# Kernel optimization log

Hardware: AMD Instinct MI355X
Metric: run time of the kernel (lower is better)

The kernel has to match this reference:

```python
import jax, jax.numpy as jnp
import numpy as np

D_MODEL = 1024
EXPAND = 2
D_INNER = EXPAND * D_MODEL  # 2048
D_STATE = 16
D_CONV = 4
DT_RANK = D_INNER  # non-int dt_rank resolves to d_inner
BATCH, SEQ = 2, 1024
EPS = 1e-5


def setup_inputs() -> dict:
    key = jax.random.key(0)
    ks = jax.random.split(key, 9)
    s = 0.02
    return {
        "x": jax.random.normal(ks[0], (BATCH, SEQ, D_MODEL), jnp.float32),
        "rms_w": jnp.ones((D_MODEL,), jnp.float32),
        "W_in": jax.random.normal(ks[1], (D_MODEL, 2 * D_INNER), jnp.float32) * s,
        "conv_w": jax.random.normal(ks[2], (D_INNER, 1, D_CONV), jnp.float32) * 0.2,
        "conv_b": jax.random.normal(ks[3], (D_INNER,), jnp.float32) * 0.02,
        "W_x": jax.random.normal(ks[4], (D_INNER, DT_RANK + 2 * D_STATE), jnp.float32) * s,
        "W_dt": jax.random.normal(ks[5], (DT_RANK, D_INNER), jnp.float32) * s,
        "A_log": jax.random.normal(ks[6], (D_INNER, D_STATE), jnp.float32),
        "W_out": jax.random.normal(ks[7], (D_INNER, D_MODEL), jnp.float32) * s,
    }


def _rmsnorm(x, w):
    var = jnp.mean(jnp.square(x), axis=-1, keepdims=True)
    return x * jax.lax.rsqrt(var + EPS) * w


def _forward(x, rms_w, W_in, conv_w, conv_b, W_x, W_dt, A_log, W_out):
    B, L, _ = x.shape
    residual = x
    xn = _rmsnorm(x, rms_w)
    xr = xn @ W_in                                  # [B,L,2*d_inner]
    xs, res = jnp.split(xr, 2, axis=-1)
    # causal depthwise conv1d: torch pads d_conv-1 both sides then slices [:L]
    xc = jnp.transpose(xs, (0, 2, 1))               # [B,d_inner,L]
    xc = jnp.pad(xc, ((0, 0), (0, 0), (D_CONV - 1, 0)))
    xc = jax.lax.conv_general_dilated(
        xc, conv_w, window_strides=(1,), padding='VALID',
        dimension_numbers=('NCH', 'OIH', 'NCH'), feature_group_count=D_INNER)
    xc = xc + conv_b[None, :, None]
    xs = jax.nn.silu(jnp.transpose(xc, (0, 2, 1)))  # [B,L,d_inner]
    x_ssm = xs @ W_x                                # [B,L,d_inner+2*d_state]
    dt, Bm, Cm = jnp.split(x_ssm, [D_INNER, D_INNER + D_STATE], axis=-1)
    dt = jax.nn.softplus(dt @ W_dt)                 # [B,L,d_inner]
    A = -jnp.exp(A_log)                             # [d_inner,d_state]
    A_disc = jnp.exp(A[None, None] * dt[..., None])            # [B,L,d_inner,N]
    Bx = dt[..., None] * Bm[:, :, None, :] * xs[..., None]     # [B,L,d_inner,N]

    def step(h, inp):
        Ad_t, Bx_t, C_t = inp                       # [B,d_inner,N],[B,d_inner,N],[B,N]
        h = Ad_t * h + Bx_t
        y = jnp.einsum('bdn,bn->bd', h, C_t)
        return h, y

    h0 = jnp.zeros((B, D_INNER, D_STATE), xs.dtype)
    _, ys = jax.lax.scan(
        step, h0,
        (jnp.transpose(A_disc, (1, 0, 2, 3)),
         jnp.transpose(Bx, (1, 0, 2, 3)),
         jnp.transpose(Cm, (1, 0, 2))))
    y = jnp.transpose(ys, (1, 0, 2))                # [B,L,d_inner]
    y = y * jax.nn.silu(res)
    out = y @ W_out
    return residual + out


def reference(x, rms_w, W_in, conv_w, conv_b, W_x, W_dt, A_log, W_out):
    return _forward(x, rms_w, W_in, conv_w, conv_b, W_x, W_dt, A_log, W_out)
```

## Files before the change

### kernel.cpp

```cpp
#include <hip/hip_runtime.h>
#include <math.h>

#define B_SZ   2
#define LSEQ   1024
#define DMODEL 1024
#define DINNER 2048
#define DSTATE 16
#define NTOK   (B_SZ * LSEQ)
#define NSSM   (DINNER + 2 * DSTATE)
#define CL     32
#define NCH    (LSEQ / CL)
#define NC     (B_SZ * DINNER)

typedef unsigned short ushort;
typedef __attribute__((ext_vector_type(8))) ushort ushort8;
typedef __attribute__((ext_vector_type(8))) __bf16 bf16x8;
typedef __attribute__((ext_vector_type(4))) float floatx4;

__device__ __forceinline__ float softplus_f(float x) {
  return (x > 20.f) ? x : __logf(1.f + __expf(x));
}
__device__ __forceinline__ float silu_f(float x) {
  return x / (1.f + __expf(-x));
}
__device__ __forceinline__ float bf2f(ushort u) {
  return __uint_as_float(((unsigned)u) << 16);
}
__device__ __forceinline__ ushort f2bf(float f) {
  unsigned u = __float_as_uint(f);
  return (ushort)((u + 0x7FFFu + ((u >> 16) & 1u)) >> 16);
}

__global__ __launch_bounds__(256) void rmsnorm_kernel(
    const float* __restrict__ x, const float* __restrict__ w,
    ushort* __restrict__ xn) {
  int row = blockIdx.x;
  const float* xrow = x + (size_t)row * DMODEL;
  float v[4];
  float ss = 0.f;
#pragma unroll
  for (int i = 0; i < 4; i++) {
    v[i] = xrow[threadIdx.x + 256 * i];
    ss += v[i] * v[i];
  }
  __shared__ float wsum[4];
  int lane = threadIdx.x & 63, wid = threadIdx.x >> 6;
#pragma unroll
  for (int off = 1; off < 64; off <<= 1) ss += __shfl_xor(ss, off);
  if (lane == 0) wsum[wid] = ss;
  __syncthreads();
  float tot = wsum[0] + wsum[1] + wsum[2] + wsum[3];
  float scale = rsqrtf(tot / (float)DMODEL + 1e-5f);
#pragma unroll
  for (int i = 0; i < 4; i++) {
    int j = threadIdx.x + 256 * i;
    xn[(size_t)row * DMODEL + j] = f2bf(v[i] * scale * w[j]);
  }
}

__global__ __launch_bounds__(256) void transpose_w(
    const float* __restrict__ W, ushort* __restrict__ Wt, int K, int N) {
  __shared__ float tile[64][65];
  int n0 = blockIdx.x * 64, k0 = blockIdx.y * 64;
  int c = threadIdx.x & 63, rb = (threadIdx.x >> 6) << 4;
#pragma unroll
  for (int i = 0; i < 16; i++) {
    int k = k0 + rb + i;
    if (k < K && n0 + c < N) tile[rb + i][c] = W[(size_t)k * N + n0 + c];
  }
  __syncthreads();
#pragma unroll
  for (int i = 0; i < 16; i++) {
    int n = n0 + rb + i;
    if (n < N && k0 + c < K)
      Wt[(size_t)n * K + k0 + c] = f2bf(tile[c][rb + i]);
  }
}

__global__ __launch_bounds__(256) void gemm_mfma(
    const ushort* __restrict__ A, int lda,
    const ushort* __restrict__ Bt, int ldb,
    int N, int K, int mode,
    void* __restrict__ C0, void* __restrict__ C1,
    const float* __restrict__ addend) {
  __shared__ ushort As[2 * 128 * 32];
  __shared__ ushort Bs[2 * 128 * 32];
  const int bm = blockIdx.y * 128, bn = blockIdx.x * 128;
  const int tid = threadIdx.x;
  const int wave = tid >> 6, lane = tid & 63;
  const int wm = (wave & 1) << 6, wn = (wave >> 1) << 6;
  const int lrow = lane & 15, quad = lane >> 4;

  const int sr = tid >> 2;
  const int q  = tid & 3;
  const int swr = (sr ^ (sr >> 2)) & 3;
  const int pq = (q ^ swr) << 3;
  const int br0 = min(bn + sr, N - 1);
  const int br1 = min(bn + sr + 64, N - 1);
  const ushort* ga0 = A + (size_t)(bm + sr) * lda + (q << 3);
  const ushort* ga1 = A + (size_t)(bm + sr + 64) * lda + (q << 3);
  const ushort* gb0 = Bt + (size_t)br0 * ldb + (q << 3);
  const ushort* gb1 = Bt + (size_t)br1 * ldb + (q << 3);

  floatx4 acc[4][4];
#pragma unroll
  for (int i = 0; i < 4; i++)
#pragma unroll
    for (int j = 0; j < 4; j++) acc[i][j] = (floatx4){0.f, 0.f, 0.f, 0.f};

  const int swf = ((lrow ^ (lrow >> 2)) & 3);
  const int fq = ((quad ^ swf) << 3);

  const int nk = K >> 5;
  ushort8 ra0 = *(const ushort8*)ga0, ra1 = *(const ushort8*)ga1;
  ushort8 rb0 = *(const ushort8*)gb0, rb1 = *(const ushort8*)gb1;
  for (int kt = 0; kt < nk; kt++) {
    const int bo = (kt & 1) << 12;
    *(ushort8*)&As[bo + sr * 32 + pq] = ra0;
    *(ushort8*)&As[bo + (sr + 64) * 32 + pq] = ra1;
    *(ushort8*)&Bs[bo + sr * 32 + pq] = rb0;
    *(ushort8*)&Bs[bo + (sr + 64) * 32 + pq] = rb1;
    __syncthreads();
    if (kt + 1 < nk) {
      const int ko = (kt + 1) << 5;
      ra0 = *(const ushort8*)(ga0 + ko);
      ra1 = *(const ushort8*)(ga1 + ko);
      rb0 = *(const ushort8*)(gb0 + ko);
      rb1 = *(const ushort8*)(gb1 + ko);
    }
    bf16x8 af[4], bfr[4];
#pragma unroll
    for (int i = 0; i < 4; i++)
      af[i] = __builtin_bit_cast(bf16x8,
          *(const ushort8*)&As[bo + (wm + i * 16 + lrow) * 32 + fq]);
#pragma unroll
    for (int j = 0; j < 4; j++)
      bfr[j] = __builtin_bit_cast(bf16x8,
          *(const ushort8*)&Bs[bo + (wn + j * 16 + lrow) * 32 + fq]);
#pragma unroll
    for (int i = 0; i < 4; i++)
#pragma unroll
      for (int j = 0; j < 4; j++)
        acc[i][j] = __builtin_amdgcn_mfma_f32_16x16x32_bf16(
            af[i], bfr[j], acc[i][j], 0, 0, 0);
  }
  const int m0 = bm + wm, n0 = bn + wn, rq = quad << 2;
#pragma unroll
  for (int i = 0; i < 4; i++) {
#pragma unroll
    for (int j = 0; j < 4; j++) {
#pragma unroll
      for (int r = 0; r < 4; r++) {
        int m = m0 + i * 16 + rq + r;
        int n = n0 + j * 16 + lrow;
        if (n >= N) continue;
        float v = acc[i][j][r];
        if (mode == 0) {
          ((float*)C0)[(size_t)m * N + n] = v + addend[(size_t)m * N + n];
        } else if (mode == 1) {
          if (n < DINNER)
            ((ushort*)C0)[(size_t)m * DINNER + n] = f2bf(v);
          else
            ((ushort*)C1)[(size_t)m * DINNER + n - DINNER] = f2bf(silu_f(v));
        } else if (mode == 2) {
          ((ushort*)C0)[(size_t)m * NSSM + n] = f2bf(v);
          if (n >= DINNER)
            ((float*)C1)[(size_t)m * 32 + n - DINNER] = v;
        } else {
          ((float*)C0)[(size_t)m * DINNER + n] = softplus_f(v);
        }
      }
    }
  }
}

__global__ __launch_bounds__(256) void conv_silu_kernel(
    const ushort* __restrict__ xsraw, const float* __restrict__ cw,
    const float* __restrict__ cb, ushort* __restrict__ xs) {
  int gid = blockIdx.x * 256 + threadIdx.x;
  int c = gid & (DINNER - 1);
  int t = gid >> 11;
  int l = t & (LSEQ - 1);
  float w0 = cw[c * 4 + 0], w1 = cw[c * 4 + 1], w2 = cw[c * 4 + 2], w3 = cw[c * 4 + 3];
  const ushort* col = xsraw + (size_t)t * DINNER + c;
  float acc = cb[c] + w3 * bf2f(col[0]);
  if (l >= 1) acc += w2 * bf2f(col[-DINNER]);
  if (l >= 2) acc += w1 * bf2f(col[-2 * DINNER]);
  if (l >= 3) acc += w0 * bf2f(col[-3 * DINNER]);
  xs[gid] = f2bf(silu_f(acc));
}

__global__ __launch_bounds__(256) void scan_chunk1(
    const float* __restrict__ dt, const ushort* __restrict__ xs,
    const float* __restrict__ bc, const float* __restrict__ A_log,
    float* __restrict__ Bc, float* __restrict__ S) {
  int blk = blockIdx.x;
  int b = blk >> 8;
  int rem = blk & 255;
  int ch = rem >> 3;
  int dblk = rem & 7;
  int d = dblk * 256 + threadIdx.x;
  int c = b * DINNER + d;
  float a[DSTATE];
#pragma unroll
  for (int i = 0; i < 4; i++) {
    float4 v = *(const float4*)(A_log + (size_t)d * DSTATE + 4 * i);
    a[4 * i + 0] = -__expf(v.x);
    a[4 * i + 1] = -__expf(v.y);
    a[4 * i + 2] = -__expf(v.z);
    a[4 * i + 3] = -__expf(v.w);
  }
  float h[DSTATE] = {};
  float Ssum = 0.f;
  size_t t = (size_t)b * LSEQ + (size_t)ch * CL;
#pragma unroll 2
  for (int l = 0; l < CL; l++, t++) {
    float dtv = dt[t * DINNER + d];
    float dx = dtv * bf2f(xs[t * DINNER + d]);
    const float4* Bp = (const float4*)(bc + t * 32);
    float4 b0 = Bp[0], b1 = Bp[1], b2 = Bp[2], b3 = Bp[3];
    float bb[DSTATE] = {b0.x, b0.y, b0.z, b0.w, b1.x, b1.y, b1.z, b1.w,
                        b2.x, b2.y, b2.z, b2.w, b3.x, b3.y, b3.z, b3.w};
#pragma unroll
    for (int n = 0; n < DSTATE; n++)
      h[n] = __expf(a[n] * dtv) * h[n] + dx * bb[n];
    Ssum += dtv;
  }
  float4* outp = (float4*)(Bc + ((size_t)c * NCH + ch) * DSTATE);
  outp[0] = make_float4(h[0], h[1], h[2], h[3]);
  outp[1] = make_float4(h[4], h[5], h[6], h[7]);
  outp[2] = make_float4(h[8], h[9], h[10], h[11]);
  outp[3] = make_float4(h[12], h[13], h[14], h[15]);
  S[c * NCH + ch] = Ssum;
}

__global__ __launch_bounds__(256) void scan_combine(
    const float* __restrict__ A_log, const float* __restrict__ S,
    float* BcHin) {
  int gid = blockIdx.x * 256 + threadIdx.x;
  int c = gid >> 4, n = gid & 15;
  int d = c & (DINNER - 1);
  float a = -__expf(A_log[d * DSTATE + n]);
  float h = 0.f;
  size_t base = (size_t)c * (NCH * DSTATE) + n;
  for (int ch = 0; ch < NCH; ch++) {
    float bcv = BcHin[base + (size_t)ch * DSTATE];
    float decay = __expf(a * S[c * NCH + ch]);
    BcHin[base + (size_t)ch * DSTATE] = h;
    h = decay * h + bcv;
  }
}

__global__ __launch_bounds__(256) void scan_chunk2(
    const float* __restrict__ dt, const ushort* __restrict__ xs,
    const float* __restrict__ bc, const ushort* __restrict__ gate,
    const float* __restrict__ A_log, const float* __restrict__ hin,
    ushort* __restrict__ y) {
  int blk = blockIdx.x;
  int b = blk >> 8;
  int rem = blk & 255;
  int ch = rem >> 3;
  int dblk = rem & 7;
  int d = dblk * 256 + threadIdx.x;
  int c = b * DINNER + d;
  float a[DSTATE];
#pragma unroll
  for (int i = 0; i < 4; i++) {
    float4 v = *(const float4*)(A_log + (size_t)d * DSTATE + 4 * i);
    a[4 * i + 0] = -__expf(v.x);
    a[4 * i + 1] = -__expf(v.y);
    a[4 * i + 2] = -__expf(v.z);
    a[4 * i + 3] = -__expf(v.w);
  }
  float h[DSTATE];
  const float4* hi = (const float4*)(hin + ((size_t)c * NCH + ch) * DSTATE);
#pragma unroll
  for (int i = 0; i < 4; i++) {
    float4 v = hi[i];
    h[4 * i + 0] = v.x; h[4 * i + 1] = v.y; h[4 * i + 2] = v.z; h[4 * i + 3] = v.w;
  }
  size_t t = (size_t)b * LSEQ + (size_t)ch * CL;
#pragma unroll 2
  for (int l = 0; l < CL; l++, t++) {
    float dtv = dt[t * DINNER + d];
    float dx = dtv * bf2f(xs[t * DINNER + d]);
    const float4* Bp = (const float4*)(bc + t * 32);
    const float4* Cp = (const float4*)(bc + t * 32 + 16);
    float4 b0 = Bp[0], b1 = Bp[1], b2 = Bp[2], b3 = Bp[3];
    float4 c0 = Cp[0], c1 = Cp[1], c2 = Cp[2], c3 = Cp[3];
    float bb[DSTATE] = {b0.x, b0.y, b0.z, b0.w, b1.x, b1.y, b1.z, b1.w,
                        b2.x, b2.y, b2.z, b2.w, b3.x, b3.y, b3.z, b3.w};
    float cc[DSTATE] = {c0.x, c0.y, c0.z, c0.w, c1.x, c1.y, c1.z, c1.w,
                        c2.x, c2.y, c2.z, c2.w, c3.x, c3.y, c3.z, c3.w};
    float ysum = 0.f;
#pragma unroll
    for (int n = 0; n < DSTATE; n++) {
      h[n] = __expf(a[n] * dtv) * h[n] + dx * bb[n];
      ysum = fmaf(h[n], cc[n], ysum);
    }
    y[t * DINNER + d] = f2bf(ysum * bf2f(gate[t * DINNER + d]));
  }
}

extern "C" void kernel_launch(void* const* d_in, const int* in_sizes, int n_in,
                              void* d_out, int out_size, void* d_ws, size_t ws_size,
                              hipStream_t stream) {
  const float* x      = (const float*)d_in[0];
  const float* rms_w  = (const float*)d_in[1];
  const float* W_in   = (const float*)d_in[2];
  const float* conv_w = (const float*)d_in[3];
  const float* conv_b = (const float*)d_in[4];
  const float* W_x    = (const float*)d_in[5];
  const float* W_dt   = (const float*)d_in[6];
  const float* A_log  = (const float*)d_in[7];
  const float* W_out  = (const float*)d_in[8];
  float* out = (float*)d_out;

  char* w = (char*)d_ws;
  ushort* xnb   = (ushort*)(w + 0);
  ushort* xsraw = (ushort*)(w + 4194304);
  ushort* gate  = (ushort*)(w + 12582912);
  ushort* xsb   = (ushort*)(w + 20971520);
  ushort* ssmb  = (ushort*)(w + 29360128);
  float*  dtb   = (float*)(w + 37879808);
  ushort* yb    = (ushort*)(w + 54657024);
  ushort* WinT  = (ushort*)(w + 63045632);
  ushort* WxT   = (ushort*)(w + 71434240);
  ushort* WdtT  = (ushort*)(w + 79953920);
  ushort* WoutT = (ushort*)(w + 88342528);
  float* bc = (float*)(w + 0);
  float* S  = (float*)(w + 262144);
  float* Bc = (float*)(w + 4194304);

  transpose_w<<<dim3(64, 16), 256, 0, stream>>>(W_in, WinT, DMODEL, 4096);
  transpose_w<<<dim3(33, 32), 256, 0, stream>>>(W_x, WxT, DINNER, NSSM);
  transpose_w<<<dim3(32, 32), 256, 0, stream>>>(W_dt, WdtT, DINNER, DINNER);
  transpose_w<<<dim3(16, 32), 256, 0, stream>>>(W_out, WoutT, DINNER, DMODEL);

  rmsnorm_kernel<<<NTOK, 256, 0, stream>>>(x, rms_w, xnb);
  gemm_mfma<<<dim3(32, 16), 256, 0, stream>>>(
      xnb, DMODEL, WinT, DMODEL, 4096, DMODEL, 1, xsraw, gate, nullptr);
  conv_silu_kernel<<<(NTOK * DINNER) / 256, 256, 0, stream>>>(xsraw, conv_w, conv_b, xsb);
  gemm_mfma<<<dim3(17, 16), 256, 0, stream>>>(
      xsb, DINNER, WxT, DINNER, NSSM, DINNER, 2, ssmb, bc, nullptr);
  gemm_mfma<<<dim3(16, 16), 256, 0, stream>>>(
      ssmb, NSSM, WdtT, DINNER, DINNER, DINNER, 3, dtb, nullptr, nullptr);
  scan_chunk1<<<B_SZ * NCH * 8, 256, 0, stream>>>(dtb, xsb, bc, A_log, Bc, S);
  scan_combine<<<(NC * DSTATE) / 256, 256, 0, stream>>>(A_log, S, Bc);
  scan_chunk2<<<B_SZ * NCH * 8, 256, 0, stream>>>(dtb, xsb, bc, gate, A_log, Bc, yb);
  gemm_mfma<<<dim3(8, 16), 256, 0, stream>>>(
      yb, DINNER, WoutT, DINNER, DMODEL, DINNER, 0, out, nullptr, x);
}
```

Before: 384.9 us.

## Split-K output GEMM, deepen GEMM K-tile, halve scan chunk, merge weight transposes

Several independent changes land together. The four weight-transpose launches become one kernel dispatched by block index. The GEMM now stages a 64-wide K slice per iteration (two 32-wide sub-tiles, doubling LDS use) with launch bounds targeting two blocks per CU. The final W_out GEMM is split along K across blockIdx.z, writing partials that a separate reduce kernel sums together with the residual. The scan chunk length halves so more blocks run in parallel. The cost is an extra partial buffer round trip, an extra launch, and more chunk state for the combine pass; workspace offsets are reshuffled to make room.

```diff
diff --git a/kernel.cpp b/kernel.cpp
--- a/kernel.cpp
+++ b/kernel.cpp
@@ -8,7 +8,7 @@
 #define DSTATE 16
 #define NTOK   (B_SZ * LSEQ)
 #define NSSM   (DINNER + 2 * DSTATE)
-#define CL     32
+#define CL     16
 #define NCH    (LSEQ / CL)
 #define NC     (B_SZ * DINNER)
 
@@ -58,10 +58,19 @@
   }
 }
 
-__global__ __launch_bounds__(256) void transpose_w(
-    const float* __restrict__ W, ushort* __restrict__ Wt, int K, int N) {
+__global__ __launch_bounds__(256) void transpose_all(
+    const float* __restrict__ Win, ushort* __restrict__ WinT,
+    const float* __restrict__ Wx, ushort* __restrict__ WxT,
+    const float* __restrict__ Wdt, ushort* __restrict__ WdtT,
+    const float* __restrict__ Wout, ushort* __restrict__ WoutT) {
+  int blk = blockIdx.x;
+  const float* W; ushort* Wt; int K, N, nb, idx;
+  if (blk < 1024)      { W = Win;  Wt = WinT;  K = DMODEL; N = 4096;  nb = 64; idx = blk; }
+  else if (blk < 2080) { W = Wx;   Wt = WxT;   K = DINNER; N = NSSM;  nb = 33; idx = blk - 1024; }
+  else if (blk < 3104) { W = Wdt;  Wt = WdtT;  K = DINNER; N = DINNER;nb = 32; idx = blk - 2080; }
+  else                 { W = Wout; Wt = WoutT; K = DINNER; N = DMODEL;nb = 16; idx = blk - 3104; }
+  int n0 = (idx % nb) * 64, k0 = (idx / nb) * 64;
   __shared__ float tile[64][65];
-  int n0 = blockIdx.x * 64, k0 = blockIdx.y * 64;
   int c = threadIdx.x & 63, rb = (threadIdx.x >> 6) << 4;
 #pragma unroll
   for (int i = 0; i < 16; i++) {
@@ -77,19 +86,20 @@
   }
 }
 
-__global__ __launch_bounds__(256) void gemm_mfma(
+__global__ __launch_bounds__(256, 2) void gemm_mfma(
     const ushort* __restrict__ A, int lda,
     const ushort* __restrict__ Bt, int ldb,
     int N, int K, int mode,
     void* __restrict__ C0, void* __restrict__ C1,
     const float* __restrict__ addend) {
-  __shared__ ushort As[2 * 128 * 32];
-  __shared__ ushort Bs[2 * 128 * 32];
+  __shared__ ushort As[2 * 2 * 128 * 32];
+  __shared__ ushort Bs[2 * 2 * 128 * 32];
   const int bm = blockIdx.y * 128, bn = blockIdx.x * 128;
   const int tid = threadIdx.x;
   const int wave = tid >> 6, lane = tid & 63;
   const int wm = (wave & 1) << 6, wn = (wave >> 1) << 6;
   const int lrow = lane & 15, quad = lane >> 4;
+  const size_t koff = (size_t)blockIdx.z * K;
 
   const int sr = tid >> 2;
   const int q  = tid & 3;
@@ -97,10 +107,10 @@
   const int pq = (q ^ swr) << 3;
   const int br0 = min(bn + sr, N - 1);
   const int br1 = min(bn + sr + 64, N - 1);
-  const ushort* ga0 = A + (size_t)(bm + sr) * lda + (q << 3);
-  const ushort* ga1 = A + (size_t)(bm + sr + 64) * lda + (q << 3);
-  const ushort* gb0 = Bt + (size_t)br0 * ldb + (q << 3);
-  const ushort* gb1 = Bt + (size_t)br1 * ldb + (q << 3);
+  const ushort* ga0 = A + (size_t)(bm + sr) * lda + koff + (q << 3);
+  const ushort* ga1 = A + (size_t)(bm + sr + 64) * lda + koff + (q << 3);
+  const ushort* gb0 = Bt + (size_t)br0 * ldb + koff + (q << 3);
+  const ushort* gb1 = Bt + (size_t)br1 * ldb + koff + (q << 3);
 
   floatx4 acc[4][4];
 #pragma unroll
@@ -111,40 +121,58 @@
   const int swf = ((lrow ^ (lrow >> 2)) & 3);
   const int fq = ((quad ^ swf) << 3);
 
-  const int nk = K >> 5;
-  ushort8 ra0 = *(const ushort8*)ga0, ra1 = *(const ushort8*)ga1;
-  ushort8 rb0 = *(const ushort8*)gb0, rb1 = *(const ushort8*)gb1;
+  const int nk = K >> 6;
+  ushort8 ra[2][2], rb[2][2];
+#pragma unroll
+  for (int p = 0; p < 2; p++) {
+    ra[p][0] = *(const ushort8*)(ga0 + p * 32);
+    ra[p][1] = *(const ushort8*)(ga1 + p * 32);
+    rb[p][0] = *(const ushort8*)(gb0 + p * 32);
+    rb[p][1] = *(const ushort8*)(gb1 + p * 32);
+  }
   for (int kt = 0; kt < nk; kt++) {
-    const int bo = (kt & 1) << 12;
-    *(ushort8*)&As[bo + sr * 32 + pq] = ra0;
-    *(ushort8*)&As[bo + (sr + 64) * 32 + pq] = ra1;
-    *(ushort8*)&Bs[bo + sr * 32 + pq] = rb0;
-    *(ushort8*)&Bs[bo + (sr + 64) * 32 + pq] = rb1;
+    const int bo = (kt & 1) << 13;
+#pragma unroll
+    for (int p = 0; p < 2; p++) {
+      const int po = bo + (p << 12);
+      *(ushort8*)&As[po + sr * 32 + pq] = ra[p][0];
+      *(ushort8*)&As[po + (sr + 64) * 32 + pq] = ra[p][1];
+      *(ushort8*)&Bs[po + sr * 32 + pq] = rb[p][0];
+      *(ushort8*)&Bs[po + (sr + 64) * 32 + pq] = rb[p][1];
+    }
     __syncthreads();
     if (kt + 1 < nk) {
-      const int ko = (kt + 1) << 5;
-      ra0 = *(const ushort8*)(ga0 + ko);
-      ra1 = *(const ushort8*)(ga1 + ko);
-      rb0 = *(const ushort8*)(gb0 + ko);
-      rb1 = *(const ushort8*)(gb1 + ko);
-    }
-    bf16x8 af[4], bfr[4];
-#pragma unroll
-    for (int i = 0; i < 4; i++)
-      af[i] = __builtin_bit_cast(bf16x8,
-          *(const ushort8*)&As[bo + (wm + i * 16 + lrow) * 32 + fq]);
-#pragma unroll
-    for (int j = 0; j < 4; j++)
-      bfr[j] = __builtin_bit_cast(bf16x8,
-          *(const ushort8*)&Bs[bo + (wn + j * 16 + lrow) * 32 + fq]);
-#pragma unroll
-    for (int i = 0; i < 4; i++)
+      const int ko = (kt + 1) << 6;
+#pragma unroll
+      for (int p = 0; p < 2; p++) {
+        ra[p][0] = *(const ushort8*)(ga0 + ko + p * 32);
+        ra[p][1] = *(const ushort8*)(ga1 + ko + p * 32);
+        rb[p][0] = *(const ushort8*)(gb0 + ko + p * 32);
+        rb[p][1] = *(const ushort8*)(gb1 + ko + p * 32);
+      }
+    }
+#pragma unroll
+    for (int p = 0; p < 2; p++) {
+      const int po = bo + (p << 12);
+      bf16x8 af[4], bfr[4];
+#pragma unroll
+      for (int i = 0; i < 4; i++)
+        af[i] = __builtin_bit_cast(bf16x8,
+            *(const ushort8*)&As[po + (wm + i * 16 + lrow) * 32 + fq]);
 #pragma unroll
       for (int j = 0; j < 4; j++)
-        acc[i][j] = __builtin_amdgcn_mfma_f32_16x16x32_bf16(
-            af[i], bfr[j], acc[i][j], 0, 0, 0);
+        bfr[j] = __builtin_bit_cast(bf16x8,
+            *(const ushort8*)&Bs[po + (wn + j * 16 + lrow) * 32 + fq]);
+#pragma unroll
+      for (int i = 0; i < 4; i++)
+#pragma unroll
+        for (int j = 0; j < 4; j++)
+          acc[i][j] = __builtin_amdgcn_mfma_f32_16x16x32_bf16(
+              af[i], bfr[j], acc[i][j], 0, 0, 0);
+    }
   }
   const int m0 = bm + wm, n0 = bn + wn, rq = quad << 2;
+  float* P = (float*)C0 + (size_t)blockIdx.z * NTOK * N;
 #pragma unroll
   for (int i = 0; i < 4; i++) {
 #pragma unroll
@@ -156,7 +184,7 @@
         if (n >= N) continue;
         float v = acc[i][j][r];
         if (mode == 0) {
-          ((float*)C0)[(size_t)m * N + n] = v + addend[(size_t)m * N + n];
+          P[(size_t)m * N + n] = v;
         } else if (mode == 1) {
           if (n < DINNER)
             ((ushort*)C0)[(size_t)m * DINNER + n] = f2bf(v);
@@ -172,6 +200,17 @@
       }
     }
   }
+}
+
+__global__ __launch_bounds__(256) void reduce_wout(
+    const float* __restrict__ P, const float* __restrict__ x,
+    float* __restrict__ out) {
+  int gid = blockIdx.x * 256 + threadIdx.x;
+  const float4 a = ((const float4*)P)[gid];
+  const float4 b = ((const float4*)P)[gid + (NTOK * DMODEL / 4)];
+  const float4 r = ((const float4*)x)[gid];
+  ((float4*)out)[gid] = make_float4(a.x + b.x + r.x, a.y + b.y + r.y,
+                                    a.z + b.z + r.z, a.w + b.w + r.w);
 }
 
 __global__ __launch_bounds__(256) void conv_silu_kernel(
@@ -195,8 +234,8 @@
     const float* __restrict__ bc, const float* __restrict__ A_log,
     float* __restrict__ Bc, float* __restrict__ S) {
   int blk = blockIdx.x;
-  int b = blk >> 8;
-  int rem = blk & 255;
+  int b = blk >> 9;
+  int rem = blk & 511;
   int ch = rem >> 3;
   int dblk = rem & 7;
   int d = dblk * 256 + threadIdx.x;
@@ -257,8 +296,8 @@
     const float* __restrict__ A_log, const float* __restrict__ hin,
     ushort* __restrict__ y) {
   int blk = blockIdx.x;
-  int b = blk >> 8;
-  int rem = blk & 255;
+  int b = blk >> 9;
+  int rem = blk & 511;
   int ch = rem >> 3;
   int dblk = rem & 7;
   int d = dblk * 256 + threadIdx.x;
@@ -329,13 +368,11 @@
   ushort* WdtT  = (ushort*)(w + 79953920);
   ushort* WoutT = (ushort*)(w + 88342528);
   float* bc = (float*)(w + 0);
-  float* S  = (float*)(w + 262144);
-  float* Bc = (float*)(w + 4194304);
-
-  transpose_w<<<dim3(64, 16), 256, 0, stream>>>(W_in, WinT, DMODEL, 4096);
-  transpose_w<<<dim3(33, 32), 256, 0, stream>>>(W_x, WxT, DINNER, NSSM);
-  transpose_w<<<dim3(32, 32), 256, 0, stream>>>(W_dt, WdtT, DINNER, DINNER);
-  transpose_w<<<dim3(16, 32), 256, 0, stream>>>(W_out, WoutT, DINNER, DMODEL);
+  float* Bc = (float*)(w + 63045632);
+  float* S  = (float*)(w + 79953920);
+  float* P  = (float*)(w + 4194304);
+
+  transpose_all<<<3616, 256, 0, stream>>>(W_in, WinT, W_x, WxT, W_dt, WdtT, W_out, WoutT);
 
   rmsnorm_kernel<<<NTOK, 256, 0, stream>>>(x, rms_w, xnb);
   gemm_mfma<<<dim3(32, 16), 256, 0, stream>>>(
@@ -348,6 +385,7 @@
   scan_chunk1<<<B_SZ * NCH * 8, 256, 0, stream>>>(dtb, xsb, bc, A_log, Bc, S);
   scan_combine<<<(NC * DSTATE) / 256, 256, 0, stream>>>(A_log, S, Bc);
   scan_chunk2<<<B_SZ * NCH * 8, 256, 0, stream>>>(dtb, xsb, bc, gate, A_log, Bc, yb);
-  gemm_mfma<<<dim3(8, 16), 256, 0, stream>>>(
-      yb, DINNER, WoutT, DINNER, DMODEL, DINNER, 0, out, nullptr, x);
-}
+  gemm_mfma<<<dim3(8, 16, 2), 256, 0, stream>>>(
+      yb, DINNER, WoutT, DINNER, DMODEL, DINNER / 2, 0, P, nullptr, nullptr);
+  reduce_wout<<<(NTOK * DMODEL / 4) / 256, 256, 0, stream>>>(P, x, out);
+}
```

Result: faster. 332.8 us (-13.5%).
